# Kernel optimization log

Hardware: AMD Instinct MI355X
Metric: run time of the kernel (lower is better)

Reference implementation:

```python
import jax, jax.numpy as jnp
import numpy as np

H = 16          # num_heads
W = 256         # sliding window size
LN_EPS = 1e-6
ROPE_BASE = 10000.0


def layer_norm(x, g, b):
    m = jnp.mean(x, axis=-1, keepdims=True)
    v = jnp.mean((x - m) ** 2, axis=-1, keepdims=True)
    return (x - m) * jax.lax.rsqrt(v + LN_EPS) * g + b


def rope(x):
    # x: [B, S, H, hd]; rotate-half RoPE
    S, hd = x.shape[1], x.shape[-1]
    inv_freq = 1.0 / (ROPE_BASE ** (jnp.arange(0, hd, 2, dtype=jnp.float32) / hd))
    ang = jnp.arange(S, dtype=jnp.float32)[:, None] * inv_freq[None, :]  # [S, hd/2]
    cos = jnp.concatenate([jnp.cos(ang), jnp.cos(ang)], axis=-1)[None, :, None, :]
    sin = jnp.concatenate([jnp.sin(ang), jnp.sin(ang)], axis=-1)[None, :, None, :]
    x1, x2 = jnp.split(x, 2, axis=-1)
    rot = jnp.concatenate([-x2, x1], axis=-1)
    return x * cos + rot * sin


def setup_inputs() -> dict:
    key = jax.random.key(0)
    ks = jax.random.split(key, 12)
    B, S, D, I = 2, 2048, 1024, 4096
    s = 0.02
    return {
        "hidden_states": jax.random.normal(ks[0], (B, S, D), jnp.float32),
        "wq": jax.random.normal(ks[1], (D, D), jnp.float32) * s,
        "wk": jax.random.normal(ks[2], (D, D), jnp.float32) * s,
        "wv": jax.random.normal(ks[3], (D, D), jnp.float32) * s,
        "wo": jax.random.normal(ks[4], (D, D), jnp.float32) * s,
        "w1": jax.random.normal(ks[5], (D, I), jnp.float32) * s,
        "w2": jax.random.normal(ks[6], (I, D), jnp.float32) * s,
        "w3": jax.random.normal(ks[7], (D, I), jnp.float32) * s,
        "ln1_g": jnp.ones((D,), jnp.float32),
        "ln1_b": jnp.zeros((D,), jnp.float32),
        "ln2_g": jnp.ones((D,), jnp.float32),
        "ln2_b": jnp.zeros((D,), jnp.float32),
    }


def reference(hidden_states, wq, wk, wv, wo, w1, w2, w3, ln1_g, ln1_b, ln2_g, ln2_b):
    B, S, D = hidden_states.shape
    hd = D // H

    # --- attention sub-block ---
    residual = hidden_states
    x = layer_norm(hidden_states, ln1_g, ln1_b)
    q = (x @ wq).reshape(B, S, H, hd)
    k = (x @ wk).reshape(B, S, H, hd)
    v = (x @ wv).reshape(B, S, H, hd)
    q, k = rope(q), rope(k)

    scores = jnp.einsum("bqhd,bkhd->bhqk", q, k) / jnp.sqrt(jnp.float32(hd))
    idx = jnp.arange(S)
    rel = idx[:, None] - idx[None, :]          # i - j
    mask = (rel >= 0) & (rel < W)              # causal sliding window
    scores = jnp.where(mask[None, None], scores, jnp.float32(-1e9))
    attn = jax.nn.softmax(scores, axis=-1)
    ctx = jnp.einsum("bhqk,bkhd->bqhd", attn, v).reshape(B, S, D)
    hidden_states = residual + ctx @ wo

    # --- SwiGLU MLP sub-block ---
    residual = hidden_states
    x = layer_norm(hidden_states, ln2_g, ln2_b)
    mlp = (jax.nn.silu(x @ w1) * (x @ w3)) @ w2
    return residual + mlp
```

## Files before the change

### kernel.cpp

```cpp
#include <hip/hip_runtime.h>
#include <hip/hip_bf16.h>

typedef __bf16 bf16_t;
typedef __bf16 bf16x4 __attribute__((ext_vector_type(4)));
typedef __bf16 bf16x8 __attribute__((ext_vector_type(8)));
typedef float f32x4 __attribute__((ext_vector_type(4)));

#define LN_EPS 1e-6f

__device__ __forceinline__ void gl2lds16(const void* g, void* l) {
    __builtin_amdgcn_global_load_lds(
        (const __attribute__((address_space(1))) void*)g,
        (__attribute__((address_space(3))) void*)l, 16, 0, 0);
}

__device__ __forceinline__ void block_sync() {
    __asm__ __volatile__("" ::: "memory");
    __builtin_amdgcn_s_barrier();
    __asm__ __volatile__("" ::: "memory");
}

__global__ void transpose_cvt_kernel(const float* __restrict__ in, bf16_t* __restrict__ out,
                                     int R, int C) {
    __shared__ float tile[32][33];
    int tx = threadIdx.x & 31;
    int ty = threadIdx.x >> 5;
    int r0 = blockIdx.y * 32;
    int c0 = blockIdx.x * 32;
#pragma unroll
    for (int i = 0; i < 4; i++) {
        int r = ty + i * 8;
        tile[r][tx] = in[(size_t)(r0 + r) * C + (c0 + tx)];
    }
    __syncthreads();
#pragma unroll
    for (int i = 0; i < 4; i++) {
        int r = ty + i * 8;
        out[(size_t)(c0 + r) * R + (r0 + tx)] = (bf16_t)tile[tx][r];
    }
}

__global__ void ln_kernel(const float* __restrict__ x, const float* __restrict__ g,
                          const float* __restrict__ bb, bf16_t* __restrict__ out, int D) {
    int row = blockIdx.x;
    int t = threadIdx.x;
    const float4* xr = reinterpret_cast<const float4*>(x + (size_t)row * D);
    float4 v = xr[t];
    float s = v.x + v.y + v.z + v.w;
    __shared__ float sbuf[4];
    __shared__ float sbuf2[4];
    int wave = t >> 6, lane = t & 63;
#pragma unroll
    for (int o = 32; o > 0; o >>= 1) s += __shfl_xor(s, o);
    if (lane == 0) sbuf[wave] = s;
    __syncthreads();
    float mean = (sbuf[0] + sbuf[1] + sbuf[2] + sbuf[3]) / (float)D;
    float d0 = v.x - mean, d1 = v.y - mean, d2 = v.z - mean, d3 = v.w - mean;
    float sq = d0 * d0 + d1 * d1 + d2 * d2 + d3 * d3;
#pragma unroll
    for (int o = 32; o > 0; o >>= 1) sq += __shfl_xor(sq, o);
    if (lane == 0) sbuf2[wave] = sq;
    __syncthreads();
    float var = (sbuf2[0] + sbuf2[1] + sbuf2[2] + sbuf2[3]) / (float)D;
    float inv = rsqrtf(var + LN_EPS);
    float4 gv = reinterpret_cast<const float4*>(g)[t];
    float4 bv = reinterpret_cast<const float4*>(bb)[t];
    bf16_t* o0 = out + (size_t)row * D + t * 4;
    o0[0] = (bf16_t)(d0 * inv * gv.x + bv.x);
    o0[1] = (bf16_t)(d1 * inv * gv.y + bv.y);
    o0[2] = (bf16_t)(d2 * inv * gv.z + bv.z);
    o0[3] = (bf16_t)(d3 * inv * gv.w + bv.w);
}

#define G4_BK 64

template <int EPI>
__launch_bounds__(256, 2) __global__
void gemm4_kernel(const bf16_t* __restrict__ A, const bf16_t* __restrict__ Bt,
                  float* __restrict__ Cf, const float* __restrict__ aux,
                  const bf16_t* __restrict__ auxb, bf16_t* __restrict__ Cb,
                  int M, int N, int K, int lda, int ldb) {
    __shared__ __align__(16) bf16_t As[128 * G4_BK];
    __shared__ __align__(16) bf16_t Bs[128 * G4_BK];
    const int t = threadIdx.x;
    const int wave = t >> 6, lane = t & 63;
    const int lr = lane & 15, quad = lane >> 4;
    const int wm = (wave >> 1) * 64, wn = (wave & 1) * 64;

    const int gx = gridDim.x, gy = gridDim.y;
    const int nwg = gx * gy;
    const int lin = blockIdx.y * gx + blockIdx.x;
    const int qch = nwg >> 3;
    const int sw = (lin & 7) * qch + (lin >> 3);
    const int m0 = (sw / gy) * 128;
    const int n0 = (sw % gy) * 128;
    const int koff = blockIdx.z * K;

    const int srow = t >> 3;
    const int sslot = (t & 7) ^ (srow & 7);
    const bf16_t* agp = A + (size_t)(m0 + srow) * lda + koff + sslot * 8;
    const bf16_t* bgp = Bt + (size_t)(n0 + srow) * ldb + koff + sslot * 8;
    bf16_t* asl = As + t * 8;
    bf16_t* bsl = Bs + t * 8;

    int aoff[4][2], boff[4][2];
#pragma unroll
    for (int f = 0; f < 4; f++)
#pragma unroll
        for (int s = 0; s < 2; s++) {
            int ra = wm + f * 16 + lr;
            int rb = wn + f * 16 + lr;
            aoff[f][s] = ra * G4_BK + (((s * 4 + quad) ^ (ra & 7)) << 3);
            boff[f][s] = rb * G4_BK + (((s * 4 + quad) ^ (rb & 7)) << 3);
        }

    f32x4 acc[4][4];
#pragma unroll
    for (int mi = 0; mi < 4; mi++)
#pragma unroll
        for (int ni = 0; ni < 4; ni++) acc[mi][ni] = 0.f;

    for (int k0 = 0; k0 < K; k0 += G4_BK) {
#pragma unroll
        for (int i = 0; i < 4; i++)
            gl2lds16(agp + k0 + (size_t)(32 * i) * lda, asl + i * 2048);
#pragma unroll
        for (int i = 0; i < 4; i++)
            gl2lds16(bgp + k0 + (size_t)(32 * i) * ldb, bsl + i * 2048);
        __syncthreads();
#pragma unroll
        for (int s = 0; s < 2; s++) {
            bf16x8 af[4], bfv[4];
#pragma unroll
            for (int mi = 0; mi < 4; mi++)
                af[mi] = *reinterpret_cast<const bf16x8*>(&As[aoff[mi][s]]);
#pragma unroll
            for (int ni = 0; ni < 4; ni++)
                bfv[ni] = *reinterpret_cast<const bf16x8*>(&Bs[boff[ni][s]]);
#pragma unroll
            for (int mi = 0; mi < 4; mi++)
#pragma unroll
                for (int ni = 0; ni < 4; ni++)
                    acc[mi][ni] = __builtin_amdgcn_mfma_f32_16x16x32_bf16(af[mi], bfv[ni],
                                                                          acc[mi][ni], 0, 0, 0);
        }
        __syncthreads();
    }

#pragma unroll
    for (int mi = 0; mi < 4; mi++)
#pragma unroll
        for (int ni = 0; ni < 4; ni++)
#pragma unroll
            for (int j = 0; j < 4; j++) {
                int gm = m0 + wm + mi * 16 + quad * 4 + j;
                int gn = n0 + wn + ni * 16 + lr;
                size_t idx = (size_t)gm * N + gn;
                float val = acc[mi][ni][j];
                if constexpr (EPI == 1) {
                    Cf[idx] = val + aux[idx];
                }
            }
}


__device__ __forceinline__ void stage_half(const bf16_t* g, int ld, bf16_t* l,
                                           int wave, int lane) {
#pragma unroll
    for (int i = 0; i < 2; i++) {
        int lidx = (wave * 2 + i) * 64 + lane;
        int row = lidx >> 3;
        int ss = (lidx & 7) ^ (row & 7);
        gl2lds16(g + (size_t)row * ld + ss * 8, l + (wave * 2 + i) * 512);
    }
}

template <int QM, int QN>
__device__ __forceinline__ void quad_mfma(f32x4 (&acc)[2][2][4][2], const bf16x8 (&af)[4][2],
                                          const bf16x8 (&bf)[2][2]) {
#pragma unroll
    for (int fr = 0; fr < 4; fr++)
#pragma unroll
        for (int fc = 0; fc < 2; fc++)
#pragma unroll
            for (int ks = 0; ks < 2; ks++)
                acc[QM][QN][fr][fc] = __builtin_amdgcn_mfma_f32_16x16x32_bf16(
                    af[fr][ks], bf[fc][ks], acc[QM][QN][fr][fc], 0, 0, 0);
}

template <int EPI>
__launch_bounds__(512, 2) __global__
void gemm5_kernel(const bf16_t* __restrict__ A, const bf16_t* __restrict__ Bt,
                  const bf16_t* __restrict__ auxb, bf16_t* __restrict__ Cb,
                  int M, int N, int K, int lda, int ldb) {
    extern __shared__ __align__(16) bf16_t smem[];
    bf16_t* smA = smem;
    bf16_t* smB = smem + 32768;
    const int t = threadIdx.x;
    const int wave = t >> 6, lane = t & 63;
    const int lr = lane & 15, quad = lane >> 4;
    const int rowgrp = wave >> 2;
    const int colgrp = wave & 3;
    const int cg1 = colgrp & 1, cg2 = colgrp >> 1;

    const int gx = gridDim.x, gy = gridDim.y;
    const int nwg = gx * gy;
    const int lin = blockIdx.y * gx + blockIdx.x;
    const int qch = nwg >> 3;
    const int sw = (lin & 7) * qch + (lin >> 3);
    const int m0 = (sw / gy) * 256;
    const int n0 = (sw % gy) * 256;
    const int koff = blockIdx.z * K;

    const bf16_t* Ag = A + (size_t)m0 * lda + koff;
    const bf16_t* Bg = Bt + (size_t)n0 * ldb + koff;

    int aoff[4][2], boff[2][2];
#pragma unroll
    for (int fr = 0; fr < 4; fr++)
#pragma unroll
        for (int ks = 0; ks < 2; ks++) {
            int ra = rowgrp * 64 + fr * 16 + lr;
            aoff[fr][ks] = ra * 64 + (((ks * 4 + quad) ^ (ra & 7)) << 3);
        }
#pragma unroll
    for (int fc = 0; fc < 2; fc++)
#pragma unroll
        for (int ks = 0; ks < 2; ks++) {
            int rb = cg1 * 64 + cg2 * 16 + fc * 32 + lr;
            boff[fc][ks] = rb * 64 + (((ks * 4 + quad) ^ (rb & 7)) << 3);
        }

    f32x4 acc[2][2][4][2];
#pragma unroll
    for (int qm = 0; qm < 2; qm++)
#pragma unroll
        for (int qn = 0; qn < 2; qn++)
#pragma unroll
            for (int fr = 0; fr < 4; fr++)
#pragma unroll
                for (int fc = 0; fc < 2; fc++) acc[qm][qn][fr][fc] = 0.f;

    stage_half(Ag, lda, smA, wave, lane);
    stage_half(Bg, ldb, smB, wave, lane);
    stage_half(Bg + (size_t)128 * ldb, ldb, smB + 8192, wave, lane);
    stage_half(Ag + (size_t)128 * lda, lda, smA + 8192, wave, lane);
    __asm__ __volatile__("s_waitcnt vmcnt(4)" ::: "memory");
    block_sync();

    const int NT = K >> 6;
    bf16x8 af[4][2], bf0[2][2], bf1[2][2];

    for (int tt = 0; tt < NT; ++tt) {
        const int cur = tt & 1, nxt = cur ^ 1;
        const bf16_t* A0b = smA + cur * 16384;
        const bf16_t* A1b = A0b + 8192;
        const bf16_t* B0b = smB + cur * 16384;
        const bf16_t* B1b = B0b + 8192;
        bf16_t* sA0n = smA + nxt * 16384;
        bf16_t* sB0n = smB + nxt * 16384;
        const bool pf = (tt + 1 < NT);
        const size_t kn = (size_t)(tt + 1) << 6;

#pragma unroll
        for (int fr = 0; fr < 4; fr++)
#pragma unroll
            for (int ks = 0; ks < 2; ks++)
                af[fr][ks] = *reinterpret_cast<const bf16x8*>(A0b + aoff[fr][ks]);
#pragma unroll
        for (int fc = 0; fc < 2; fc++)
#pragma unroll
            for (int ks = 0; ks < 2; ks++)
                bf0[fc][ks] = *reinterpret_cast<const bf16x8*>(B0b + boff[fc][ks]);
        if (pf) {
            stage_half(Ag + kn, lda, sA0n, wave, lane);
            stage_half(Bg + kn, ldb, sB0n, wave, lane);
        }
        block_sync();
        __asm__ __volatile__("s_waitcnt lgkmcnt(0)" ::: "memory");
        __builtin_amdgcn_sched_barrier(0);
        __builtin_amdgcn_s_setprio(1);
        quad_mfma<0, 0>(acc, af, bf0);
        __builtin_amdgcn_s_setprio(0);
        __asm__ __volatile__("s_waitcnt vmcnt(6)" ::: "memory");
        block_sync();

#pragma unroll
        for (int fc = 0; fc < 2; fc++)
#pragma unroll
            for (int ks = 0; ks < 2; ks++)
                bf1[fc][ks] = *reinterpret_cast<const bf16x8*>(B1b + boff[fc][ks]);
        if (pf) stage_half(Bg + (size_t)128 * ldb + kn, ldb, sB0n + 8192, wave, lane);
        block_sync();
        __asm__ __volatile__("s_waitcnt lgkmcnt(0)" ::: "memory");
        __builtin_amdgcn_sched_barrier(0);
        __builtin_amdgcn_s_setprio(1);
        quad_mfma<0, 1>(acc, af, bf1);
        __builtin_amdgcn_s_setprio(0);
        __asm__ __volatile__("s_waitcnt vmcnt(6)" ::: "memory");
        block_sync();

#pragma unroll
        for (int fr = 0; fr < 4; fr++)
#pragma unroll
            for (int ks = 0; ks < 2; ks++)
                af[fr][ks] = *reinterpret_cast<const bf16x8*>(A1b + aoff[fr][ks]);
        if (pf) stage_half(Ag + (size_t)128 * lda + kn, lda, sA0n + 8192, wave, lane);
        block_sync();
        __asm__ __volatile__("s_waitcnt lgkmcnt(0)" ::: "memory");
        __builtin_amdgcn_sched_barrier(0);
        __builtin_amdgcn_s_setprio(1);
        quad_mfma<1, 1>(acc, af, bf1);
        quad_mfma<1, 0>(acc, af, bf0);
        __builtin_amdgcn_s_setprio(0);
        __asm__ __volatile__("s_waitcnt vmcnt(4)" ::: "memory");
        block_sync();
    }

    if constexpr (EPI == 3) {
        const float kfreq = -0.41524101186f;
        bool do_rope = (n0 + 128 < 2048 + 1);
        const int d = cg2 * 16 + lr;
        const float freq = exp2f((float)d * kfreq);
#pragma unroll
        for (int qm = 0; qm < 2; qm++)
#pragma unroll
            for (int qn = 0; qn < 2; qn++) {
                const int gnb = n0 + qn * 128 + cg1 * 64;
#pragma unroll
                for (int fr = 0; fr < 4; fr++)
#pragma unroll
                    for (int j = 0; j < 4; j++) {
                        int gm = m0 + qm * 128 + rowgrp * 64 + fr * 16 + quad * 4 + j;
                        if (do_rope) {
                            float pos = (float)(gm & 2047);
                            float ang = pos * freq;
                            float sn, cs;
                            __sincosf(ang, &sn, &cs);
                            float x1 = acc[qm][qn][fr][0][j];
                            float x2 = acc[qm][qn][fr][1][j];
                            size_t idx = (size_t)gm * N + gnb + d;
                            Cb[idx] = (bf16_t)(x1 * cs - x2 * sn);
                            Cb[idx + 32] = (bf16_t)(x2 * cs + x1 * sn);
                        } else {
#pragma unroll
                            for (int fc = 0; fc < 2; fc++) {
                                size_t idx = (size_t)gm * N + gnb + cg2 * 16 + fc * 32 + lr;
                                Cb[idx] = (bf16_t)acc[qm][qn][fr][fc][j];
                            }
                        }
                    }
            }
    } else {
        size_t outoff = (EPI == 5) ? (size_t)blockIdx.z * M * N : 0;
#pragma unroll
        for (int qm = 0; qm < 2; qm++)
#pragma unroll
            for (int qn = 0; qn < 2; qn++)
#pragma unroll
                for (int fr = 0; fr < 4; fr++)
#pragma unroll
                    for (int fc = 0; fc < 2; fc++)
#pragma unroll
                        for (int j = 0; j < 4; j++) {
                            int gm = m0 + qm * 128 + rowgrp * 64 + fr * 16 + quad * 4 + j;
                            int gn = n0 + qn * 128 + cg1 * 64 + cg2 * 16 + fc * 32 + lr;
                            size_t idx = (size_t)gm * N + gn;
                            float val = acc[qm][qn][fr][fc][j];
                            if constexpr (EPI == 2) {
                                float a = (float)auxb[idx];
                                float sl = a / (1.0f + __expf(-a));
                                Cb[idx] = (bf16_t)(sl * val);
                            } else if constexpr (EPI == 4) {
                                Cb[idx] = (bf16_t)val;
                            } else if constexpr (EPI == 5) {
                                Cb[outoff + idx] = (bf16_t)val;
                            }
                        }
    }
}

__global__ void reduce4_kernel(const bf16_t* __restrict__ p, const float* __restrict__ hid,
                               float* __restrict__ out, int n4) {
    int i = blockIdx.x * 256 + threadIdx.x;
    if (i >= n4) return;
    size_t i4 = (size_t)i * 4;
    float4 h = *reinterpret_cast<const float4*>(hid + i4);
    const size_t stride = (size_t)4096 * 1024;
#pragma unroll
    for (int c = 0; c < 4; c++) {
        bf16x4 a = *reinterpret_cast<const bf16x4*>(p + c * stride + i4);
        h.x += (float)a[0];
        h.y += (float)a[1];
        h.z += (float)a[2];
        h.w += (float)a[3];
    }
    *reinterpret_cast<float4*>(out + i4) = h;
}

__global__ void transpose_v_kernel(const bf16_t* __restrict__ v, bf16_t* __restrict__ vt,
                                   int S, int stride) {
    __shared__ bf16_t tile[64][66];
    int t = threadIdx.x;
    int s0 = blockIdx.x * 64;
    int h = blockIdx.y, b = blockIdx.z;
#pragma unroll
    for (int i = 0; i < 2; i++) {
        int c = t + i * 256;
        int ss = c >> 3, d8 = (c & 7) * 8;
        bf16x8 val = *reinterpret_cast<const bf16x8*>(
            &v[(size_t)(b * S + s0 + ss) * stride + h * 64 + d8]);
#pragma unroll
        for (int jj = 0; jj < 8; jj++) tile[ss][d8 + jj] = val[jj];
    }
    __syncthreads();
#pragma unroll
    for (int i = 0; i < 2; i++) {
        int c = t + i * 256;
        int d = c >> 3, s8 = (c & 7) * 8;
        bf16x8 o;
#pragma unroll
        for (int jj = 0; jj < 8; jj++) o[jj] = tile[s8 + jj][d];
        *reinterpret_cast<bf16x8*>(&vt[(((size_t)(b * 16 + h)) * 64 + d) * S + s0 + s8]) = o;
    }
}

#define PSTR 40
#define QKVS 3072
__global__ __launch_bounds__(256, 2) void attn_kernel(const bf16_t* __restrict__ qkv,
                                                      const bf16_t* __restrict__ vt,
                                                      bf16_t* __restrict__ ctx, int S) {
    __shared__ __align__(16) bf16_t Pbuf[4][16 * PSTR];
    int t = threadIdx.x;
    int wave = t >> 6, lane = t & 63;
    int col = lane & 15, quad = lane >> 4;
    int h = blockIdx.y, b = blockIdx.z;
    int q0 = blockIdx.x * 64 + wave * 16;

    const bf16_t* qrow = qkv + (size_t)(b * S + q0 + col) * QKVS + h * 64;
    bf16x8 aq0 = *reinterpret_cast<const bf16x8*>(qrow + quad * 8);
    bf16x8 aq1 = *reinterpret_cast<const bf16x8*>(qrow + 32 + quad * 8);

    int jbase = q0 - 256;
    f32x4 sc[18];
#pragma unroll
    for (int kt = 0; kt < 18; kt++) {
        int j = jbase + kt * 16 + col;
        int jc = j < 0 ? 0 : (j > S - 1 ? S - 1 : j);
        const bf16_t* krow = qkv + (size_t)(b * S + jc) * QKVS + 1024 + h * 64;
        bf16x8 bk0 = *reinterpret_cast<const bf16x8*>(krow + quad * 8);
        bf16x8 bk1 = *reinterpret_cast<const bf16x8*>(krow + 32 + quad * 8);
        f32x4 c0 = {0.f, 0.f, 0.f, 0.f};
        c0 = __builtin_amdgcn_mfma_f32_16x16x32_bf16(aq0, bk0, c0, 0, 0, 0);
        c0 = __builtin_amdgcn_mfma_f32_16x16x32_bf16(aq1, bk1, c0, 0, 0, 0);
        sc[kt] = c0;
    }
#pragma unroll
    for (int kt = 0; kt < 18; kt++) {
#pragma unroll
        for (int jj = 0; jj < 4; jj++) {
            int qq = quad * 4 + jj;
            int j = jbase + kt * 16 + col;
            int rel = (q0 + qq) - j;
            bool ok = (j >= 0) && (rel >= 0) && (rel < 256);
            sc[kt][jj] = ok ? sc[kt][jj] * 0.125f : -1e30f;
        }
    }
    float sminv[4];
#pragma unroll
    for (int jj = 0; jj < 4; jj++) {
        float m = -1e30f;
#pragma unroll
        for (int kt = 0; kt < 18; kt++) m = fmaxf(m, sc[kt][jj]);
#pragma unroll
        for (int o = 1; o < 16; o <<= 1) m = fmaxf(m, __shfl_xor(m, o));
        float s = 0.f;
#pragma unroll
        for (int kt = 0; kt < 18; kt++) {
            float p = __expf(sc[kt][jj] - m);
            sc[kt][jj] = p;
            s += p;
        }
#pragma unroll
        for (int o = 1; o < 16; o <<= 1) s += __shfl_xor(s, o);
        sminv[jj] = 1.0f / s;
    }
    f32x4 o[4];
#pragma unroll
    for (int n = 0; n < 4; n++) o[n] = 0.f;
    bf16_t* myP = Pbuf[wave];
    const bf16_t* vplane = vt + ((size_t)(b * 16 + h)) * 64 * S;
#pragma unroll
    for (int c = 0; c < 9; c++) {
#pragma unroll
        for (int half = 0; half < 2; half++) {
            int kt = 2 * c + half;
#pragma unroll
            for (int jj = 0; jj < 4; jj++) {
                int qq = quad * 4 + jj;
                myP[qq * PSTR + half * 16 + col] = (bf16_t)(sc[kt][jj] * sminv[jj]);
            }
        }
        bf16x8 ap = *reinterpret_cast<const bf16x8*>(myP + col * PSTR + quad * 8);
        int key0 = jbase + c * 32 + quad * 8;
        int kc = key0 < 0 ? 0 : (key0 > S - 8 ? S - 8 : key0);
#pragma unroll
        for (int n = 0; n < 4; n++) {
            bf16x8 bv = *reinterpret_cast<const bf16x8*>(vplane + ((size_t)(n * 16 + col)) * S + kc);
            o[n] = __builtin_amdgcn_mfma_f32_16x16x32_bf16(ap, bv, o[n], 0, 0, 0);
        }
    }
#pragma unroll
    for (int n = 0; n < 4; n++)
#pragma unroll
        for (int jj = 0; jj < 4; jj++) {
            int qq = quad * 4 + jj;
            ctx[((size_t)(b * S + q0 + qq) * 16 + h) * 64 + n * 16 + col] = (bf16_t)o[n][jj];
        }
}

extern "C" void kernel_launch(void* const* d_in, const int* in_sizes, int n_in,
                              void* d_out, int out_size, void* d_ws, size_t ws_size,
                              hipStream_t stream) {
    const float* hs   = (const float*)d_in[0];
    const float* wq   = (const float*)d_in[1];
    const float* wk   = (const float*)d_in[2];
    const float* wv   = (const float*)d_in[3];
    const float* wo   = (const float*)d_in[4];
    const float* w1   = (const float*)d_in[5];
    const float* w2   = (const float*)d_in[6];
    const float* w3   = (const float*)d_in[7];
    const float* ln1g = (const float*)d_in[8];
    const float* ln1b = (const float*)d_in[9];
    const float* ln2g = (const float*)d_in[10];
    const float* ln2b = (const float*)d_in[11];
    float* out = (float*)d_out;

    const int B = 2, S = 2048, D = 1024, I = 4096;
    const int BS = B * S;

    char* ws = (char*)d_ws;
    const size_t MB = 1024 * 1024;
    bf16_t* wq_t = (bf16_t*)(ws + 0 * MB);
    bf16_t* wk_t = (bf16_t*)(ws + 2 * MB);
    bf16_t* wv_t = (bf16_t*)(ws + 4 * MB);
    bf16_t* wo_t = (bf16_t*)(ws + 6 * MB);
    bf16_t* w1_t = (bf16_t*)(ws + 8 * MB);
    bf16_t* w3_t = (bf16_t*)(ws + 16 * MB);
    bf16_t* w2_t = (bf16_t*)(ws + 24 * MB);
    bf16_t* x_b  = (bf16_t*)(ws + 32 * MB);
    float*  hid  = (float*)(ws + 40 * MB);
    bf16_t* x2_b = (bf16_t*)(ws + 56 * MB);
    bf16_t* qkvb = (bf16_t*)(ws + 64 * MB);
    bf16_t* vt   = (bf16_t*)(ws + 88 * MB);
    bf16_t* ctxb = (bf16_t*)(ws + 96 * MB);
    bf16_t* h1b  = (bf16_t*)(ws + 64 * MB);
    bf16_t* hbuf = (bf16_t*)(ws + 96 * MB);
    bf16_t* pker = (bf16_t*)(ws + 64 * MB);

    hipFuncSetAttribute(reinterpret_cast<const void*>(&gemm5_kernel<2>),
                        hipFuncAttributeMaxDynamicSharedMemorySize, 131072);
    hipFuncSetAttribute(reinterpret_cast<const void*>(&gemm5_kernel<3>),
                        hipFuncAttributeMaxDynamicSharedMemorySize, 131072);
    hipFuncSetAttribute(reinterpret_cast<const void*>(&gemm5_kernel<4>),
                        hipFuncAttributeMaxDynamicSharedMemorySize, 131072);
    hipFuncSetAttribute(reinterpret_cast<const void*>(&gemm5_kernel<5>),
                        hipFuncAttributeMaxDynamicSharedMemorySize, 131072);

    dim3 tb(256);
    dim3 tb5(512);
    transpose_cvt_kernel<<<dim3(D / 32, D / 32), tb, 0, stream>>>(wq, wq_t, D, D);
    transpose_cvt_kernel<<<dim3(D / 32, D / 32), tb, 0, stream>>>(wk, wk_t, D, D);
    transpose_cvt_kernel<<<dim3(D / 32, D / 32), tb, 0, stream>>>(wv, wv_t, D, D);
    transpose_cvt_kernel<<<dim3(D / 32, D / 32), tb, 0, stream>>>(wo, wo_t, D, D);
    transpose_cvt_kernel<<<dim3(I / 32, D / 32), tb, 0, stream>>>(w1, w1_t, D, I);
    transpose_cvt_kernel<<<dim3(I / 32, D / 32), tb, 0, stream>>>(w3, w3_t, D, I);
    transpose_cvt_kernel<<<dim3(D / 32, I / 32), tb, 0, stream>>>(w2, w2_t, I, D);

    ln_kernel<<<BS, tb, 0, stream>>>(hs, ln1g, ln1b, x_b, D);

    gemm5_kernel<3><<<dim3(BS / 256, 3072 / 256), tb5, 131072, stream>>>(
        x_b, wq_t, nullptr, qkvb, BS, 3072, D, D, D);

    transpose_v_kernel<<<dim3(S / 64, 16, B), tb, 0, stream>>>(qkvb + 2048, vt, S, QKVS);

    attn_kernel<<<dim3(S / 64, 16, B), tb, 0, stream>>>(qkvb, vt, ctxb, S);

    gemm4_kernel<1><<<dim3(BS / 128, D / 128), tb, 0, stream>>>(
        ctxb, wo_t, hid, hs, nullptr, nullptr, BS, D, D, D, D);

    ln_kernel<<<BS, tb, 0, stream>>>(hid, ln2g, ln2b, x2_b, D);

    gemm5_kernel<4><<<dim3(BS / 256, I / 256), tb5, 131072, stream>>>(
        x2_b, w1_t, nullptr, h1b, BS, I, D, D, D);
    gemm5_kernel<2><<<dim3(BS / 256, I / 256), tb5, 131072, stream>>>(
        x2_b, w3_t, h1b, hbuf, BS, I, D, D, D);

    gemm5_kernel<5><<<dim3(BS / 256, D / 256, 4), tb5, 131072, stream>>>(
        hbuf, w2_t, nullptr, pker, BS, D, 1024, I, I);
    reduce4_kernel<<<dim3(BS * D / 4 / 256), tb, 0, stream>>>(pker, hid, out, BS * D / 4);
}
```

Measured before the change: 379.6 us.

## Fuse w1/w3 GEMMs with SwiGLU epilogue, fold V transpose into QKV GEMM

The w1 and w3 weights are interleaved in 128-column blocks, so one GEMM computes both the gate and the up projection per tile and applies SiLU-multiply in registers. This removes the intermediate h1 buffer write and re-read and one launch. The QKV GEMM epilogue now writes V directly in transposed layout, which removes the separate transpose kernel. The seven weight-prep transposes are merged into one launch. The attention kernel also scans 17 key tiles instead of 18, padding the extra P slot with zeros to skip one fully masked tile. In exchange, the transposed V stores are strided 4-element writes and the weight-prep kernel has extra index logic.

```diff
diff --git a/kernel.cpp b/kernel.cpp
--- a/kernel.cpp
+++ b/kernel.cpp
@@ -20,23 +20,48 @@
     __asm__ __volatile__("" ::: "memory");
 }
 
-__global__ void transpose_cvt_kernel(const float* __restrict__ in, bf16_t* __restrict__ out,
-                                     int R, int C) {
+__global__ void prep_weights_kernel(const float* __restrict__ wq, const float* __restrict__ wk,
+                                    const float* __restrict__ wv, const float* __restrict__ wo,
+                                    const float* __restrict__ w1, const float* __restrict__ w3,
+                                    const float* __restrict__ w2, bf16_t* __restrict__ wq_t,
+                                    bf16_t* __restrict__ wk_t, bf16_t* __restrict__ wv_t,
+                                    bf16_t* __restrict__ wo_t, bf16_t* __restrict__ w13_t,
+                                    bf16_t* __restrict__ w2_t) {
     __shared__ float tile[32][33];
+    int id = blockIdx.x;
+    const float* src;
+    bf16_t* dst;
+    int R, C, mode = 0;
+    if (id < 4096) {
+        int w = id >> 10;
+        id &= 1023;
+        src = (w == 0) ? wq : (w == 1) ? wk : (w == 2) ? wv : wo;
+        dst = (w == 0) ? wq_t : (w == 1) ? wk_t : (w == 2) ? wv_t : wo_t;
+        R = 1024; C = 1024;
+    } else if (id < 8192) {
+        id -= 4096; src = w1; dst = w13_t; R = 1024; C = 4096; mode = 1;
+    } else if (id < 12288) {
+        id -= 8192; src = w3; dst = w13_t; R = 1024; C = 4096; mode = 2;
+    } else {
+        id -= 12288; src = w2; dst = w2_t; R = 4096; C = 1024;
+    }
+    int tpc = C >> 5;
+    int bx = id % tpc, by = id / tpc;
+    int r0 = by * 32, c0 = bx * 32;
     int tx = threadIdx.x & 31;
     int ty = threadIdx.x >> 5;
-    int r0 = blockIdx.y * 32;
-    int c0 = blockIdx.x * 32;
 #pragma unroll
     for (int i = 0; i < 4; i++) {
         int r = ty + i * 8;
-        tile[r][tx] = in[(size_t)(r0 + r) * C + (c0 + tx)];
+        tile[r][tx] = src[(size_t)(r0 + r) * C + (c0 + tx)];
     }
     __syncthreads();
 #pragma unroll
     for (int i = 0; i < 4; i++) {
         int r = ty + i * 8;
-        out[(size_t)(c0 + r) * R + (r0 + tx)] = (bf16_t)tile[tx][r];
+        int rr = c0 + r;
+        if (mode) rr = ((rr >> 7) << 8) + (rr & 127) + ((mode == 2) ? 128 : 0);
+        dst[(size_t)rr * R + (r0 + tx)] = (bf16_t)tile[tx][r];
     }
 }
 
@@ -192,7 +217,7 @@
 __launch_bounds__(512, 2) __global__
 void gemm5_kernel(const bf16_t* __restrict__ A, const bf16_t* __restrict__ Bt,
                   const bf16_t* __restrict__ auxb, bf16_t* __restrict__ Cb,
-                  int M, int N, int K, int lda, int ldb) {
+                  bf16_t* __restrict__ Cb2, int M, int N, int K, int lda, int ldb) {
     extern __shared__ __align__(16) bf16_t smem[];
     bf16_t* smA = smem;
     bf16_t* smB = smem + 32768;
@@ -318,21 +343,20 @@
     }
 
     if constexpr (EPI == 3) {
-        const float kfreq = -0.41524101186f;
-        bool do_rope = (n0 + 128 < 2048 + 1);
-        const int d = cg2 * 16 + lr;
-        const float freq = exp2f((float)d * kfreq);
-#pragma unroll
-        for (int qm = 0; qm < 2; qm++)
-#pragma unroll
-            for (int qn = 0; qn < 2; qn++) {
-                const int gnb = n0 + qn * 128 + cg1 * 64;
-#pragma unroll
-                for (int fr = 0; fr < 4; fr++)
-#pragma unroll
-                    for (int j = 0; j < 4; j++) {
-                        int gm = m0 + qm * 128 + rowgrp * 64 + fr * 16 + quad * 4 + j;
-                        if (do_rope) {
+        if (n0 < 2048) {
+            const float kfreq = -0.41524101186f;
+            const int d = cg2 * 16 + lr;
+            const float freq = exp2f((float)d * kfreq);
+#pragma unroll
+            for (int qm = 0; qm < 2; qm++)
+#pragma unroll
+                for (int qn = 0; qn < 2; qn++) {
+                    const int gnb = n0 + qn * 128 + cg1 * 64;
+#pragma unroll
+                    for (int fr = 0; fr < 4; fr++)
+#pragma unroll
+                        for (int j = 0; j < 4; j++) {
+                            int gm = m0 + qm * 128 + rowgrp * 64 + fr * 16 + quad * 4 + j;
                             float pos = (float)(gm & 2047);
                             float ang = pos * freq;
                             float sn, cs;
@@ -342,15 +366,45 @@
                             size_t idx = (size_t)gm * N + gnb + d;
                             Cb[idx] = (bf16_t)(x1 * cs - x2 * sn);
                             Cb[idx + 32] = (bf16_t)(x2 * cs + x1 * sn);
-                        } else {
-#pragma unroll
-                            for (int fc = 0; fc < 2; fc++) {
-                                size_t idx = (size_t)gm * N + gnb + cg2 * 16 + fc * 32 + lr;
-                                Cb[idx] = (bf16_t)acc[qm][qn][fr][fc][j];
-                            }
                         }
+                }
+        } else {
+#pragma unroll
+            for (int qm = 0; qm < 2; qm++)
+#pragma unroll
+                for (int qn = 0; qn < 2; qn++)
+#pragma unroll
+                    for (int fr = 0; fr < 4; fr++)
+#pragma unroll
+                        for (int fc = 0; fc < 2; fc++) {
+                            int gmb = m0 + qm * 128 + rowgrp * 64 + fr * 16 + quad * 4;
+                            int vcol = (n0 - 2048) + qn * 128 + cg1 * 64 + cg2 * 16 + fc * 32 + lr;
+                            int hh = vcol >> 6, dd = vcol & 63;
+                            int bb2 = gmb >> 11, ss = gmb & 2047;
+                            bf16x4 pk;
+#pragma unroll
+                            for (int j = 0; j < 4; j++) pk[j] = (bf16_t)acc[qm][qn][fr][fc][j];
+                            *reinterpret_cast<bf16x4*>(
+                                &Cb2[(((size_t)(bb2 * 16 + hh)) * 64 + dd) * 2048 + ss]) = pk;
+                        }
+        }
+    } else if constexpr (EPI == 6) {
+        const int No = N >> 1;
+#pragma unroll
+        for (int qm = 0; qm < 2; qm++)
+#pragma unroll
+            for (int fr = 0; fr < 4; fr++)
+#pragma unroll
+                for (int fc = 0; fc < 2; fc++)
+#pragma unroll
+                    for (int j = 0; j < 4; j++) {
+                        int gm = m0 + qm * 128 + rowgrp * 64 + fr * 16 + quad * 4 + j;
+                        int c = (n0 >> 1) + cg1 * 64 + cg2 * 16 + fc * 32 + lr;
+                        float a = acc[qm][0][fr][fc][j];
+                        float bv = acc[qm][1][fr][fc][j];
+                        float sl = a / (1.0f + __expf(-a));
+                        Cb[(size_t)gm * No + c] = (bf16_t)(sl * bv);
                     }
-            }
     } else {
         size_t outoff = (EPI == 5) ? (size_t)blockIdx.z * M * N : 0;
 #pragma unroll
@@ -367,14 +421,10 @@
                             int gn = n0 + qn * 128 + cg1 * 64 + cg2 * 16 + fc * 32 + lr;
                             size_t idx = (size_t)gm * N + gn;
                             float val = acc[qm][qn][fr][fc][j];
-                            if constexpr (EPI == 2) {
-                                float a = (float)auxb[idx];
-                                float sl = a / (1.0f + __expf(-a));
-                                Cb[idx] = (bf16_t)(sl * val);
-                            } else if constexpr (EPI == 4) {
+                            if constexpr (EPI == 5) {
+                                Cb[outoff + idx] = (bf16_t)val;
+                            } else {
                                 Cb[idx] = (bf16_t)val;
-                            } else if constexpr (EPI == 5) {
-                                Cb[outoff + idx] = (bf16_t)val;
                             }
                         }
     }
@@ -396,33 +446,6 @@
         h.w += (float)a[3];
     }
     *reinterpret_cast<float4*>(out + i4) = h;
-}
-
-__global__ void transpose_v_kernel(const bf16_t* __restrict__ v, bf16_t* __restrict__ vt,
-                                   int S, int stride) {
-    __shared__ bf16_t tile[64][66];
-    int t = threadIdx.x;
-    int s0 = blockIdx.x * 64;
-    int h = blockIdx.y, b = blockIdx.z;
-#pragma unroll
-    for (int i = 0; i < 2; i++) {
-        int c = t + i * 256;
-        int ss = c >> 3, d8 = (c & 7) * 8;
-        bf16x8 val = *reinterpret_cast<const bf16x8*>(
-            &v[(size_t)(b * S + s0 + ss) * stride + h * 64 + d8]);
-#pragma unroll
-        for (int jj = 0; jj < 8; jj++) tile[ss][d8 + jj] = val[jj];
-    }
-    __syncthreads();
-#pragma unroll
-    for (int i = 0; i < 2; i++) {
-        int c = t + i * 256;
-        int d = c >> 3, s8 = (c & 7) * 8;
-        bf16x8 o;
-#pragma unroll
-        for (int jj = 0; jj < 8; jj++) o[jj] = tile[s8 + jj][d];
-        *reinterpret_cast<bf16x8*>(&vt[(((size_t)(b * 16 + h)) * 64 + d) * S + s0 + s8]) = o;
-    }
 }
 
 #define PSTR 40
@@ -442,9 +465,9 @@
     bf16x8 aq1 = *reinterpret_cast<const bf16x8*>(qrow + 32 + quad * 8);
 
     int jbase = q0 - 256;
-    f32x4 sc[18];
-#pragma unroll
-    for (int kt = 0; kt < 18; kt++) {
+    f32x4 sc[17];
+#pragma unroll
+    for (int kt = 0; kt < 17; kt++) {
         int j = jbase + kt * 16 + col;
         int jc = j < 0 ? 0 : (j > S - 1 ? S - 1 : j);
         const bf16_t* krow = qkv + (size_t)(b * S + jc) * QKVS + 1024 + h * 64;
@@ -456,7 +479,7 @@
         sc[kt] = c0;
     }
 #pragma unroll
-    for (int kt = 0; kt < 18; kt++) {
+    for (int kt = 0; kt < 17; kt++) {
 #pragma unroll
         for (int jj = 0; jj < 4; jj++) {
             int qq = quad * 4 + jj;
@@ -471,12 +494,12 @@
     for (int jj = 0; jj < 4; jj++) {
         float m = -1e30f;
 #pragma unroll
-        for (int kt = 0; kt < 18; kt++) m = fmaxf(m, sc[kt][jj]);
+        for (int kt = 0; kt < 17; kt++) m = fmaxf(m, sc[kt][jj]);
 #pragma unroll
         for (int o = 1; o < 16; o <<= 1) m = fmaxf(m, __shfl_xor(m, o));
         float s = 0.f;
 #pragma unroll
-        for (int kt = 0; kt < 18; kt++) {
+        for (int kt = 0; kt < 17; kt++) {
             float p = __expf(sc[kt][jj] - m);
             sc[kt][jj] = p;
             s += p;
@@ -498,7 +521,9 @@
 #pragma unroll
             for (int jj = 0; jj < 4; jj++) {
                 int qq = quad * 4 + jj;
-                myP[qq * PSTR + half * 16 + col] = (bf16_t)(sc[kt][jj] * sminv[jj]);
+                bf16_t pv = (kt < 17) ? (bf16_t)(sc[kt < 17 ? kt : 0][jj] * sminv[jj])
+                                      : (bf16_t)0.f;
+                myP[qq * PSTR + half * 16 + col] = pv;
             }
         }
         bf16x8 ap = *reinterpret_cast<const bf16x8*>(myP + col * PSTR + quad * 8);
@@ -541,48 +566,38 @@
 
     char* ws = (char*)d_ws;
     const size_t MB = 1024 * 1024;
-    bf16_t* wq_t = (bf16_t*)(ws + 0 * MB);
-    bf16_t* wk_t = (bf16_t*)(ws + 2 * MB);
-    bf16_t* wv_t = (bf16_t*)(ws + 4 * MB);
-    bf16_t* wo_t = (bf16_t*)(ws + 6 * MB);
-    bf16_t* w1_t = (bf16_t*)(ws + 8 * MB);
-    bf16_t* w3_t = (bf16_t*)(ws + 16 * MB);
-    bf16_t* w2_t = (bf16_t*)(ws + 24 * MB);
-    bf16_t* x_b  = (bf16_t*)(ws + 32 * MB);
-    float*  hid  = (float*)(ws + 40 * MB);
-    bf16_t* x2_b = (bf16_t*)(ws + 56 * MB);
-    bf16_t* qkvb = (bf16_t*)(ws + 64 * MB);
-    bf16_t* vt   = (bf16_t*)(ws + 88 * MB);
-    bf16_t* ctxb = (bf16_t*)(ws + 96 * MB);
-    bf16_t* h1b  = (bf16_t*)(ws + 64 * MB);
-    bf16_t* hbuf = (bf16_t*)(ws + 96 * MB);
-    bf16_t* pker = (bf16_t*)(ws + 64 * MB);
-
-    hipFuncSetAttribute(reinterpret_cast<const void*>(&gemm5_kernel<2>),
-                        hipFuncAttributeMaxDynamicSharedMemorySize, 131072);
+    bf16_t* wq_t  = (bf16_t*)(ws + 0 * MB);
+    bf16_t* wk_t  = (bf16_t*)(ws + 2 * MB);
+    bf16_t* wv_t  = (bf16_t*)(ws + 4 * MB);
+    bf16_t* wo_t  = (bf16_t*)(ws + 6 * MB);
+    bf16_t* w13_t = (bf16_t*)(ws + 8 * MB);
+    bf16_t* w2_t  = (bf16_t*)(ws + 24 * MB);
+    bf16_t* x_b   = (bf16_t*)(ws + 32 * MB);
+    float*  hid   = (float*)(ws + 40 * MB);
+    bf16_t* x2_b  = (bf16_t*)(ws + 56 * MB);
+    bf16_t* qkvb  = (bf16_t*)(ws + 64 * MB);
+    bf16_t* vt    = (bf16_t*)(ws + 88 * MB);
+    bf16_t* ctxb  = (bf16_t*)(ws + 96 * MB);
+    bf16_t* hbuf  = (bf16_t*)(ws + 96 * MB);
+    bf16_t* pker  = (bf16_t*)(ws + 64 * MB);
+
     hipFuncSetAttribute(reinterpret_cast<const void*>(&gemm5_kernel<3>),
-                        hipFuncAttributeMaxDynamicSharedMemorySize, 131072);
-    hipFuncSetAttribute(reinterpret_cast<const void*>(&gemm5_kernel<4>),
                         hipFuncAttributeMaxDynamicSharedMemorySize, 131072);
     hipFuncSetAttribute(reinterpret_cast<const void*>(&gemm5_kernel<5>),
                         hipFuncAttributeMaxDynamicSharedMemorySize, 131072);
+    hipFuncSetAttribute(reinterpret_cast<const void*>(&gemm5_kernel<6>),
+                        hipFuncAttributeMaxDynamicSharedMemorySize, 131072);
 
     dim3 tb(256);
     dim3 tb5(512);
-    transpose_cvt_kernel<<<dim3(D / 32, D / 32), tb, 0, stream>>>(wq, wq_t, D, D);
-    transpose_cvt_kernel<<<dim3(D / 32, D / 32), tb, 0, stream>>>(wk, wk_t, D, D);
-    transpose_cvt_kernel<<<dim3(D / 32, D / 32), tb, 0, stream>>>(wv, wv_t, D, D);
-    transpose_cvt_kernel<<<dim3(D / 32, D / 32), tb, 0, stream>>>(wo, wo_t, D, D);
-    transpose_cvt_kernel<<<dim3(I / 32, D / 32), tb, 0, stream>>>(w1, w1_t, D, I);
-    transpose_cvt_kernel<<<dim3(I / 32, D / 32), tb, 0, stream>>>(w3, w3_t, D, I);
-    transpose_cvt_kernel<<<dim3(D / 32, I / 32), tb, 0, stream>>>(w2, w2_t, I, D);
+
+    prep_weights_kernel<<<dim3(16384), tb, 0, stream>>>(wq, wk, wv, wo, w1, w3, w2, wq_t, wk_t,
+                                                        wv_t, wo_t, w13_t, w2_t);
 
     ln_kernel<<<BS, tb, 0, stream>>>(hs, ln1g, ln1b, x_b, D);
 
     gemm5_kernel<3><<<dim3(BS / 256, 3072 / 256), tb5, 131072, stream>>>(
-        x_b, wq_t, nullptr, qkvb, BS, 3072, D, D, D);
-
-    transpose_v_kernel<<<dim3(S / 64, 16, B), tb, 0, stream>>>(qkvb + 2048, vt, S, QKVS);
+        x_b, wq_t, nullptr, qkvb, vt, BS, 3072, D, D, D);
 
     attn_kernel<<<dim3(S / 64, 16, B), tb, 0, stream>>>(qkvb, vt, ctxb, S);
 
@@ -591,12 +606,10 @@
 
     ln_kernel<<<BS, tb, 0, stream>>>(hid, ln2g, ln2b, x2_b, D);
 
-    gemm5_kernel<4><<<dim3(BS / 256, I / 256), tb5, 131072, stream>>>(
-        x2_b, w1_t, nullptr, h1b, BS, I, D, D, D);
-    gemm5_kernel<2><<<dim3(BS / 256, I / 256), tb5, 131072, stream>>>(
-        x2_b, w3_t, h1b, hbuf, BS, I, D, D, D);
+    gemm5_kernel<6><<<dim3(BS / 256, 8192 / 256), tb5, 131072, stream>>>(
+        x2_b, w13_t, nullptr, hbuf, nullptr, BS, 8192, D, D, D);
 
     gemm5_kernel<5><<<dim3(BS / 256, D / 256, 4), tb5, 131072, stream>>>(
-        hbuf, w2_t, nullptr, pker, BS, D, 1024, I, I);
+        hbuf, w2_t, nullptr, pker, nullptr, BS, D, 1024, I, I);
     reduce4_kernel<<<dim3(BS * D / 4 / 256), tb, 0, stream>>>(pker, hid, out, BS * D / 4);
 }
```

Result: faster. 357.7 us (-5.8%).
